# Performance work log

Measured on AMD Instinct MI355X. Metric: run time of the kernel, lower is better.

## Reference

```python
import jax, jax.numpy as jnp
import numpy as np

EMBED = 768
HEADS = 12
HEAD_DIM = EMBED // HEADS
HIDDEN = 4 * EMBED
EPS = 1e-5


def setup_inputs() -> dict:
    key = jax.random.key(0)
    ks = jax.random.split(key, 12)
    s = lambda fan_in: 1.0 / np.sqrt(fan_in)
    return {
        "x": jax.random.normal(ks[0], (4, 2048, EMBED), dtype=jnp.float32),
        "ln1_g": jnp.ones((EMBED,), jnp.float32),
        "ln1_b": jnp.zeros((EMBED,), jnp.float32),
        "qkv_w": jax.random.normal(ks[1], (EMBED, 3 * EMBED), jnp.float32) * s(EMBED),
        "qkv_b": jnp.zeros((3 * EMBED,), jnp.float32),
        "proj_w": jax.random.normal(ks[2], (EMBED, EMBED), jnp.float32) * s(EMBED),
        "proj_b": jnp.zeros((EMBED,), jnp.float32),
        "ln2_g": jnp.ones((EMBED,), jnp.float32),
        "ln2_b": jnp.zeros((EMBED,), jnp.float32),
        "fc1_w": jax.random.normal(ks[3], (EMBED, HIDDEN), jnp.float32) * s(EMBED),
        "fc1_b": jnp.zeros((HIDDEN,), jnp.float32),
        "fc2_w": jax.random.normal(ks[4], (HIDDEN, EMBED), jnp.float32) * s(HIDDEN),
        "fc2_b": jnp.zeros((EMBED,), jnp.float32),
    }


def _layernorm(x, g, b):
    mu = jnp.mean(x, axis=-1, keepdims=True)
    var = jnp.var(x, axis=-1, keepdims=True)
    return (x - mu) * jax.lax.rsqrt(var + EPS) * g + b


def reference(x, ln1_g, ln1_b, qkv_w, qkv_b, proj_w, proj_b,
              ln2_g, ln2_b, fc1_w, fc1_b, fc2_w, fc2_b):
    B, N, C = x.shape
    # --- attention (pre-LN) ---
    xn = _layernorm(x, ln1_g, ln1_b)
    qkv = xn @ qkv_w + qkv_b                       # [B,N,3C]
    qkv = qkv.reshape(B, N, 3, HEADS, HEAD_DIM)
    q, k, v = jnp.moveaxis(qkv, 2, 0)              # each [B,N,H,D]
    q = jnp.swapaxes(q, 1, 2)                      # [B,H,N,D]
    k = jnp.swapaxes(k, 1, 2)
    v = jnp.swapaxes(v, 1, 2)
    scale = HEAD_DIM ** -0.5
    attn = jax.nn.softmax(jnp.einsum('bhnd,bhmd->bhnm', q, k) * scale, axis=-1)
    out = jnp.einsum('bhnm,bhmd->bhnd', attn, v)   # [B,H,N,D]
    out = jnp.swapaxes(out, 1, 2).reshape(B, N, C)
    out = out @ proj_w + proj_b
    x = x + out
    # --- MLP (pre-LN) ---
    xn2 = _layernorm(x, ln2_g, ln2_b)
    h = jax.nn.gelu(xn2 @ fc1_w + fc1_b, approximate=False)
    x = x + (h @ fc2_w + fc2_b)
    return x
```

## Files before the change

kernel.cpp:

```cpp
#include <hip/hip_runtime.h>

typedef unsigned short ushort_t;
typedef __attribute__((ext_vector_type(8))) unsigned short ushort8;
typedef __attribute__((ext_vector_type(4))) unsigned short ushort4v;
typedef __attribute__((ext_vector_type(2))) unsigned int uint2v;
typedef __attribute__((ext_vector_type(4))) float f32x4;
typedef __attribute__((ext_vector_type(8))) __bf16 bf16x8;

#define DEVFN static __device__ __forceinline__

DEVFN unsigned short f2bf(float f) {
    unsigned int u = __builtin_bit_cast(unsigned int, f);
    u += 0x7FFFu + ((u >> 16) & 1u);
    return (unsigned short)(u >> 16);
}

DEVFN bf16x8 ldsfrag(const ushort_t* p) {
    ushort8 u = *reinterpret_cast<const ushort8*>(p);
    return __builtin_bit_cast(bf16x8, u);
}

DEVFN bf16x8 ldg8(const ushort_t* p) {
    ushort8 u = *reinterpret_cast<const ushort8*>(p);
    return __builtin_bit_cast(bf16x8, u);
}

DEVFN f32x4 mfma16(bf16x8 a, bf16x8 b, f32x4 c) {
    return __builtin_amdgcn_mfma_f32_16x16x32_bf16(a, b, c, 0, 0, 0);
}

DEVFN void gl2lds16(const ushort_t* g, ushort_t* l) {
    __builtin_amdgcn_global_load_lds(
        (const __attribute__((address_space(1))) unsigned int*)g,
        (__attribute__((address_space(3))) unsigned int*)l, 16, 0, 0);
}

DEVFN unsigned int cvtpk(float lo, float hi) {
    unsigned int r;
    asm("v_cvt_pk_bf16_f32 %0, %1, %2" : "=v"(r) : "v"(lo), "v"(hi));
    return r;
}

__global__ __launch_bounds__(256) void wt_kernel(const float* __restrict__ in,
                                                 ushort_t* __restrict__ out,
                                                 int K, int N) {
    __shared__ float t[32][33];
    const int n0 = blockIdx.x * 32, k0 = blockIdx.y * 32;
    const int tx = threadIdx.x & 31, ty = threadIdx.x >> 5;
    for (int j = 0; j < 4; j++)
        t[ty + 8 * j][tx] = in[(size_t)(k0 + ty + 8 * j) * N + n0 + tx];
    __syncthreads();
    for (int j = 0; j < 4; j++)
        out[(size_t)(n0 + ty + 8 * j) * K + k0 + tx] = f2bf(t[tx][ty + 8 * j]);
}

__global__ __launch_bounds__(256) void ln_kernel(const float* __restrict__ x,
                                                 const float* __restrict__ g,
                                                 const float* __restrict__ bta,
                                                 ushort_t* __restrict__ out) {
    const int row = blockIdx.x;
    const int tid = threadIdx.x;
    const float* xr = x + (size_t)row * 768;
    float v0 = xr[tid], v1 = xr[tid + 256], v2 = xr[tid + 512];
    float s = v0 + v1 + v2;
    float q = v0 * v0 + v1 * v1 + v2 * v2;
    for (int d = 32; d; d >>= 1) {
        s += __shfl_down(s, d);
        q += __shfl_down(q, d);
    }
    __shared__ float red[8];
    const int w = tid >> 6, lane = tid & 63;
    if (lane == 0) { red[w] = s; red[4 + w] = q; }
    __syncthreads();
    if (tid == 0) {
        float ts = red[0] + red[1] + red[2] + red[3];
        float tq = red[4] + red[5] + red[6] + red[7];
        float mu = ts * (1.0f / 768.0f);
        float var = tq * (1.0f / 768.0f) - mu * mu;
        red[0] = mu;
        red[1] = rsqrtf(var + 1e-5f);
    }
    __syncthreads();
    const float mu = red[0], rs = red[1];
    ushort_t* orow = out + (size_t)row * 768;
    orow[tid]       = f2bf((v0 - mu) * rs * g[tid]       + bta[tid]);
    orow[tid + 256] = f2bf((v1 - mu) * rs * g[tid + 256] + bta[tid + 256]);
    orow[tid + 512] = f2bf((v2 - mu) * rs * g[tid + 512] + bta[tid + 512]);
}

enum { EPI_QKV = 0, EPI_RES = 1, EPI_GELU = 2 };

template <int EPI, int BN>
__global__ __launch_bounds__(256) void gemm_kernel(
    const ushort_t* __restrict__ A, const ushort_t* __restrict__ BT,
    const float* __restrict__ bias, const float* __restrict__ resid,
    float* __restrict__ outf, ushort_t* __restrict__ outb,
    ushort_t* __restrict__ vtout, int M, int N, int K) {
    constexpr int NT = BN / 32;
    constexpr int BIW = BN / 32;
    __shared__ __align__(16) ushort_t As[128 * 64];
    __shared__ __align__(16) ushort_t Bs[BN * 64];
    const int bn = blockIdx.x, bm = blockIdx.y;
    const int tid = threadIdx.x;
    const int lane = tid & 63, w = tid >> 6;
    const int wm = (w >> 1) * 64, wn = (w & 1) * (BN / 2);
    const int l15 = lane & 15, l4 = lane >> 4;

    const int srow8 = lane >> 3;
    const int scol = ((lane & 7) ^ srow8) * 8;

    const ushort_t* gA = A + (size_t)(bm * 128 + w * 32 + srow8) * K + scol;
    ushort_t* lA = As + (w * 32) * 64;
    const ushort_t* gB = BT + (size_t)(bn * BN + w * (BN / 4) + srow8) * K + scol;
    ushort_t* lB = Bs + (w * (BN / 4)) * 64;

    const int sw7 = l15 & 7;
    const int aoff0 = (wm + l15) * 64 + ((l4 ^ sw7) * 8);
    const int aoff1 = (wm + l15) * 64 + (((4 + l4) ^ sw7) * 8);
    const int boff0 = (wn + l15) * 64 + ((l4 ^ sw7) * 8);
    const int boff1 = (wn + l15) * 64 + (((4 + l4) ^ sw7) * 8);

    f32x4 acc[4][NT] = {};

    for (int k0 = 0; k0 < K; k0 += 64) {
        __syncthreads();
#pragma unroll
        for (int i = 0; i < 4; i++)
            gl2lds16(gA + k0 + (size_t)i * 8 * K, lA + i * 512);
#pragma unroll
        for (int i = 0; i < BIW; i++)
            gl2lds16(gB + k0 + (size_t)i * 8 * K, lB + i * 512);
        __syncthreads();
#pragma unroll
        for (int kk = 0; kk < 2; kk++) {
            const int ao = kk ? aoff1 : aoff0;
            const int bo = kk ? boff1 : boff0;
            bf16x8 af[4], bfr[NT];
#pragma unroll
            for (int mt = 0; mt < 4; mt++)
                af[mt] = ldsfrag(As + ao + mt * 1024);
#pragma unroll
            for (int nt = 0; nt < NT; nt++)
                bfr[nt] = ldsfrag(Bs + bo + nt * 1024);
#pragma unroll
            for (int mt = 0; mt < 4; mt++)
#pragma unroll
                for (int nt = 0; nt < NT; nt++)
                    acc[mt][nt] = mfma16(bfr[nt], af[mt], acc[mt][nt]);
        }
    }

#pragma unroll
    for (int nt = 0; nt < NT; nt++) {
        const int gc0 = bn * BN + wn + nt * 16 + l4 * 4;
        const f32x4 bi = *reinterpret_cast<const f32x4*>(bias + gc0);
#pragma unroll
        for (int mt = 0; mt < 4; mt++) {
            const int gr = bm * 128 + wm + mt * 16 + l15;
            f32x4 v = acc[mt][nt] + bi;
            if constexpr (EPI == EPI_QKV) {
                if (gc0 < 768) v *= 0.18033688011f;
                if (gc0 >= 1536) {
                    const int d = gc0 - 1536;
                    const int h = d >> 6, dh = d & 63;
                    const int b = gr >> 11, tl = gr & 2047;
                    ushort_t* vrow = vtout + ((size_t)((b * 12 + h) * 64 + dh)) * 2048 + tl;
                    vrow[0]        = f2bf(v[0]);
                    vrow[2048]     = f2bf(v[1]);
                    vrow[2 * 2048] = f2bf(v[2]);
                    vrow[3 * 2048] = f2bf(v[3]);
                } else {
                    ushort4v o;
#pragma unroll
                    for (int r = 0; r < 4; r++) o[r] = f2bf(v[r]);
                    *reinterpret_cast<ushort4v*>(outb + (size_t)gr * N + gc0) = o;
                }
            } else if constexpr (EPI == EPI_RES) {
                const f32x4 rsd = *reinterpret_cast<const f32x4*>(resid + (size_t)gr * N + gc0);
                *reinterpret_cast<f32x4*>(outf + (size_t)gr * N + gc0) = v + rsd;
            } else {
                ushort4v o;
#pragma unroll
                for (int r = 0; r < 4; r++) {
                    const float gl = 0.5f * v[r] * (1.0f + erff(v[r] * 0.70710678118f));
                    o[r] = f2bf(gl);
                }
                *reinterpret_cast<ushort4v*>(outb + (size_t)gr * N + gc0) = o;
            }
        }
    }
}

__global__ __launch_bounds__(256, 4) void attn_kernel(const ushort_t* __restrict__ qkv,
                                                      const ushort_t* __restrict__ vt,
                                                      ushort_t* __restrict__ out) {
    __shared__ __align__(16) ushort_t Kb[2][4096];
    __shared__ __align__(16) ushort_t Vb[2][4096];
    __shared__ __align__(16) ushort_t Ps[4][1024];

    const int bid = blockIdx.x;
    const int nid = (bid & 7) * 192 + (bid >> 3);
    const int qt = nid & 31;
    const int bh = nid >> 5;
    const int b = bh / 12, h = bh % 12;
    const int tid = threadIdx.x;
    const int lane = tid & 63, w = tid >> 6;
    const int l15 = lane & 15, l4 = lane >> 4;

    const ushort_t* qrow = qkv + (size_t)(b * 2048 + qt * 64 + w * 16 + l15) * 2304 + h * 64;
    const bf16x8 aq0 = ldg8(qrow + l4 * 8);
    const bf16x8 aq1 = ldg8(qrow + 32 + l4 * 8);

    const int jr0 = w * 16 + (lane >> 3);
    const int jr1 = jr0 + 8;
    const int c0 = ((lane & 7) ^ (jr0 & 7)) * 8;
    const int c1 = ((lane & 7) ^ (jr1 & 7)) * 8;
    const ushort_t* kg0 = qkv + (size_t)(b * 2048 + jr0) * 2304 + 768 + h * 64 + c0;
    const ushort_t* kg1 = qkv + (size_t)(b * 2048 + jr1) * 2304 + 768 + h * 64 + c1;
    const ushort_t* vg0 = vt + (size_t)(bh * 64 + jr0) * 2048 + c0;
    const ushort_t* vg1 = vt + (size_t)(bh * 64 + jr1) * 2048 + c1;

    const int sw7 = l15 & 7;
    const int ka0 = l15 * 64 + ((l4 ^ sw7) * 8);
    const int ka1 = l15 * 64 + (((4 + l4) ^ sw7) * 8);

    ushort_t* const psw = Ps[w];
    const int pw_m = l15 & 14;
    int pwoff[4];
#pragma unroll
    for (int jt = 0; jt < 4; jt++) pwoff[jt] = l15 * 64 + (((jt * 4 + l4) ^ pw_m) * 4);
    const int pr0 = l15 * 64 + (((2 * l4) ^ pw_m) * 4);
    const int pr1 = l15 * 64 + (((8 + 2 * l4) ^ pw_m) * 4);

    float lrun = 0.f;
    f32x4 oacc[4] = {};

    gl2lds16(kg0, &Kb[0][w * 1024]);
    gl2lds16(kg1, &Kb[0][w * 1024 + 512]);
    gl2lds16(vg0, &Vb[0][w * 1024]);
    gl2lds16(vg1, &Vb[0][w * 1024 + 512]);
    __syncthreads();

    for (int kt = 0; kt < 32; kt++) {
        const int cur = kt & 1;
        if (kt < 31) {
            const size_t ko = (size_t)(kt + 1) * 64 * 2304;
            const int vo = (kt + 1) * 64;
            gl2lds16(kg0 + ko, &Kb[cur ^ 1][w * 1024]);
            gl2lds16(kg1 + ko, &Kb[cur ^ 1][w * 1024 + 512]);
            gl2lds16(vg0 + vo, &Vb[cur ^ 1][w * 1024]);
            gl2lds16(vg1 + vo, &Vb[cur ^ 1][w * 1024 + 512]);
        }
        const ushort_t* kb = Kb[cur];
        const ushort_t* vb = Vb[cur];

        f32x4 st[4];
        __builtin_amdgcn_s_setprio(1);
#pragma unroll
        for (int jt = 0; jt < 4; jt++) {
            f32x4 z = {};
            z = mfma16(ldsfrag(kb + ka0 + jt * 1024), aq0, z);
            z = mfma16(ldsfrag(kb + ka1 + jt * 1024), aq1, z);
            st[jt] = z;
        }
        __builtin_amdgcn_s_setprio(0);

        float rs = 0.f;
#pragma unroll
        for (int jt = 0; jt < 4; jt++) {
            const float p0 = __builtin_amdgcn_exp2f(st[jt][0]);
            const float p1 = __builtin_amdgcn_exp2f(st[jt][1]);
            const float p2 = __builtin_amdgcn_exp2f(st[jt][2]);
            const float p3 = __builtin_amdgcn_exp2f(st[jt][3]);
            rs += (p0 + p1) + (p2 + p3);
            uint2v pw;
            pw[0] = cvtpk(p0, p1);
            pw[1] = cvtpk(p2, p3);
            *reinterpret_cast<uint2v*>(psw + pwoff[jt]) = pw;
        }
        lrun += rs;

        const bf16x8 pf0 = ldsfrag(psw + pr0);
        const bf16x8 pf1 = ldsfrag(psw + pr1);

        __builtin_amdgcn_s_setprio(1);
#pragma unroll
        for (int dt = 0; dt < 4; dt++) {
            const bf16x8 vf0 = ldsfrag(vb + ka0 + dt * 1024);
            const bf16x8 vf1 = ldsfrag(vb + ka1 + dt * 1024);
            oacc[dt] = mfma16(vf0, pf0, oacc[dt]);
            oacc[dt] = mfma16(vf1, pf1, oacc[dt]);
        }
        __builtin_amdgcn_s_setprio(0);
        __syncthreads();
    }

    lrun += __shfl_xor(lrun, 16);
    lrun += __shfl_xor(lrun, 32);
    const float linv = __builtin_amdgcn_rcpf(lrun);

    ushort_t* orow = out + (size_t)(b * 2048 + qt * 64 + w * 16 + l15) * 768 + h * 64 + l4 * 4;
#pragma unroll
    for (int dt = 0; dt < 4; dt++) {
        ushort4v o;
#pragma unroll
        for (int r = 0; r < 4; r++) o[r] = f2bf(oacc[dt][r] * linv);
        *reinterpret_cast<ushort4v*>(orow + dt * 16) = o;
    }
}

extern "C" void kernel_launch(void* const* d_in, const int* in_sizes, int n_in,
                              void* d_out, int out_size, void* d_ws, size_t ws_size,
                              hipStream_t stream) {
    const float* x      = (const float*)d_in[0];
    const float* ln1_g  = (const float*)d_in[1];
    const float* ln1_b  = (const float*)d_in[2];
    const float* qkv_w  = (const float*)d_in[3];
    const float* qkv_b  = (const float*)d_in[4];
    const float* proj_w = (const float*)d_in[5];
    const float* proj_b = (const float*)d_in[6];
    const float* ln2_g  = (const float*)d_in[7];
    const float* ln2_b  = (const float*)d_in[8];
    const float* fc1_w  = (const float*)d_in[9];
    const float* fc1_b  = (const float*)d_in[10];
    const float* fc2_w  = (const float*)d_in[11];
    const float* fc2_b  = (const float*)d_in[12];
    float* out = (float*)d_out;

    char* ws = (char*)d_ws;
    ushort_t* qkv_wt  = (ushort_t*)(ws);
    ushort_t* proj_wt = (ushort_t*)(ws + 3538944);
    ushort_t* fc1_wt  = (ushort_t*)(ws + 4718592);
    ushort_t* fc2_wt  = (ushort_t*)(ws + 9437184);
    ushort_t* xb      = (ushort_t*)(ws + 14155776);
    ushort_t* aob     = (ushort_t*)(ws + 26738688);
    ushort_t* qkvb    = (ushort_t*)(ws + 39321600);
    ushort_t* vtb     = (ushort_t*)(ws + 77070336);
    ushort_t* hb      = (ushort_t*)(ws + 39321600);

    dim3 blk(256);

    wt_kernel<<<dim3(72, 24), blk, 0, stream>>>(qkv_w, qkv_wt, 768, 2304);
    wt_kernel<<<dim3(24, 24), blk, 0, stream>>>(proj_w, proj_wt, 768, 768);
    wt_kernel<<<dim3(96, 24), blk, 0, stream>>>(fc1_w, fc1_wt, 768, 3072);
    wt_kernel<<<dim3(24, 96), blk, 0, stream>>>(fc2_w, fc2_wt, 3072, 768);

    ln_kernel<<<8192, blk, 0, stream>>>(x, ln1_g, ln1_b, xb);
    gemm_kernel<EPI_QKV, 128><<<dim3(18, 64), blk, 0, stream>>>(
        xb, qkv_wt, qkv_b, nullptr, nullptr, qkvb, vtb, 8192, 2304, 768);
    attn_kernel<<<dim3(1536), blk, 0, stream>>>(qkvb, vtb, aob);
    gemm_kernel<EPI_RES, 64><<<dim3(12, 64), blk, 0, stream>>>(
        aob, proj_wt, proj_b, x, out, nullptr, nullptr, 8192, 768, 768);
    ln_kernel<<<8192, blk, 0, stream>>>(out, ln2_g, ln2_b, xb);
    gemm_kernel<EPI_GELU, 128><<<dim3(24, 64), blk, 0, stream>>>(
        xb, fc1_wt, fc1_b, nullptr, nullptr, hb, nullptr, 8192, 3072, 768);
    gemm_kernel<EPI_RES, 64><<<dim3(12, 64), blk, 0, stream>>>(
        hb, fc2_wt, fc2_b, out, out, nullptr, nullptr, 8192, 768, 3072);
}
```

Baseline: 315.5 us.

## Double-buffer GEMM LDS tiles, fuse weight transposes, use fast GELU and packed bf16 stores

The GEMM kernel now keeps two LDS stages and issues the next k-tile's global-to-LDS loads before computing the current one, so memory latency can overlap with MFMA work. BK becomes a template parameter, set to 32 for the wide GEMMs to limit LDS use. The four weight-transpose launches are merged into one kernel to cut launch overhead. The GELU epilogue switches from erf to a tanh approximation built from exp2/rcp, and bf16 stores use packed hardware conversion. The tanh GELU changes numerics slightly relative to the exact erf reference.

```diff
diff --git a/kernel.cpp b/kernel.cpp
--- a/kernel.cpp
+++ b/kernel.cpp
@@ -41,11 +41,32 @@
     return r;
 }
 
-__global__ __launch_bounds__(256) void wt_kernel(const float* __restrict__ in,
-                                                 ushort_t* __restrict__ out,
-                                                 int K, int N) {
+DEVFN float gelu_fast(float v) {
+    const float a = 0.7978845608f * v * fmaf(0.044715f, v * v, 1.0f);
+    const float e = __builtin_amdgcn_exp2f(2.885390082f * a);
+    const float th = 1.0f - 2.0f * __builtin_amdgcn_rcpf(e + 1.0f);
+    return 0.5f * v * (1.0f + th);
+}
+
+__global__ __launch_bounds__(256) void wt4_kernel(
+    const float* __restrict__ qkv_w, const float* __restrict__ proj_w,
+    const float* __restrict__ fc1_w, const float* __restrict__ fc2_w,
+    ushort_t* __restrict__ qkv_wt, ushort_t* __restrict__ proj_wt,
+    ushort_t* __restrict__ fc1_wt, ushort_t* __restrict__ fc2_wt) {
     __shared__ float t[32][33];
-    const int n0 = blockIdx.x * 32, k0 = blockIdx.y * 32;
+    const int bid = blockIdx.x;
+    const float* in; ushort_t* out; int K, N, n0, k0;
+    if (bid < 1728)      { in = qkv_w;  out = qkv_wt;  K = 768;  N = 2304;
+                           n0 = (bid % 72) * 32;  k0 = (bid / 72) * 32; }
+    else if (bid < 2304) { const int r = bid - 1728; in = proj_w; out = proj_wt;
+                           K = 768;  N = 768;
+                           n0 = (r % 24) * 32;    k0 = (r / 24) * 32; }
+    else if (bid < 4608) { const int r = bid - 2304; in = fc1_w;  out = fc1_wt;
+                           K = 768;  N = 3072;
+                           n0 = (r % 96) * 32;    k0 = (r / 96) * 32; }
+    else                 { const int r = bid - 4608; in = fc2_w;  out = fc2_wt;
+                           K = 3072; N = 768;
+                           n0 = (r % 24) * 32;    k0 = (r / 24) * 32; }
     const int tx = threadIdx.x & 31, ty = threadIdx.x >> 5;
     for (int j = 0; j < 4; j++)
         t[ty + 8 * j][tx] = in[(size_t)(k0 + ty + 8 * j) * N + n0 + tx];
@@ -90,64 +111,72 @@
 
 enum { EPI_QKV = 0, EPI_RES = 1, EPI_GELU = 2 };
 
-template <int EPI, int BN>
+template <int EPI, int BN, int BK>
 __global__ __launch_bounds__(256) void gemm_kernel(
     const ushort_t* __restrict__ A, const ushort_t* __restrict__ BT,
     const float* __restrict__ bias, const float* __restrict__ resid,
     float* __restrict__ outf, ushort_t* __restrict__ outb,
     ushort_t* __restrict__ vtout, int M, int N, int K) {
     constexpr int NT = BN / 32;
-    constexpr int BIW = BN / 32;
-    __shared__ __align__(16) ushort_t As[128 * 64];
-    __shared__ __align__(16) ushort_t Bs[BN * 64];
+    constexpr int SL = BK / 8;
+    constexpr int SM = SL - 1;
+    constexpr int RPI = 64 / SL;
+    constexpr int AI = 128 / RPI / 4;
+    constexpr int BI = BN / RPI / 4;
+    __shared__ __align__(16) ushort_t As[2][128 * BK];
+    __shared__ __align__(16) ushort_t Bs[2][BN * BK];
     const int bn = blockIdx.x, bm = blockIdx.y;
     const int tid = threadIdx.x;
     const int lane = tid & 63, w = tid >> 6;
     const int wm = (w >> 1) * 64, wn = (w & 1) * (BN / 2);
     const int l15 = lane & 15, l4 = lane >> 4;
 
-    const int srow8 = lane >> 3;
-    const int scol = ((lane & 7) ^ srow8) * 8;
-
-    const ushort_t* gA = A + (size_t)(bm * 128 + w * 32 + srow8) * K + scol;
-    ushort_t* lA = As + (w * 32) * 64;
-    const ushort_t* gB = BT + (size_t)(bn * BN + w * (BN / 4) + srow8) * K + scol;
-    ushort_t* lB = Bs + (w * (BN / 4)) * 64;
-
-    const int sw7 = l15 & 7;
-    const int aoff0 = (wm + l15) * 64 + ((l4 ^ sw7) * 8);
-    const int aoff1 = (wm + l15) * 64 + (((4 + l4) ^ sw7) * 8);
-    const int boff0 = (wn + l15) * 64 + ((l4 ^ sw7) * 8);
-    const int boff1 = (wn + l15) * 64 + (((4 + l4) ^ sw7) * 8);
+    const int srow = lane / SL;
+    const int scol = ((lane & SM) ^ (srow & SM)) * 8;
+    const ushort_t* gA = A + (size_t)(bm * 128 + w * (AI * RPI) + srow) * K + scol;
+    const ushort_t* gB = BT + (size_t)(bn * BN + w * (BI * RPI) + srow) * K + scol;
+
+    const int swm = l15 & SM;
+    int aoff[BK / 32], boff[BK / 32];
+#pragma unroll
+    for (int kk = 0; kk < BK / 32; kk++) {
+        aoff[kk] = (wm + l15) * BK + ((((kk << 2) | l4) ^ swm) * 8);
+        boff[kk] = (wn + l15) * BK + ((((kk << 2) | l4) ^ swm) * 8);
+    }
 
     f32x4 acc[4][NT] = {};
 
-    for (int k0 = 0; k0 < K; k0 += 64) {
-        __syncthreads();
-#pragma unroll
-        for (int i = 0; i < 4; i++)
-            gl2lds16(gA + k0 + (size_t)i * 8 * K, lA + i * 512);
-#pragma unroll
-        for (int i = 0; i < BIW; i++)
-            gl2lds16(gB + k0 + (size_t)i * 8 * K, lB + i * 512);
-        __syncthreads();
-#pragma unroll
-        for (int kk = 0; kk < 2; kk++) {
-            const int ao = kk ? aoff1 : aoff0;
-            const int bo = kk ? boff1 : boff0;
+    auto stage = [&](int k0, int buf) {
+#pragma unroll
+        for (int i = 0; i < AI; i++)
+            gl2lds16(gA + k0 + i * RPI * K, &As[buf][(w * AI + i) * 512]);
+#pragma unroll
+        for (int i = 0; i < BI; i++)
+            gl2lds16(gB + k0 + i * RPI * K, &Bs[buf][(w * BI + i) * 512]);
+    };
+
+    stage(0, 0);
+    __syncthreads();
+    int cur = 0;
+    for (int k0 = 0; k0 < K; k0 += BK) {
+        if (k0 + BK < K) stage(k0 + BK, cur ^ 1);
+#pragma unroll
+        for (int kk = 0; kk < BK / 32; kk++) {
             bf16x8 af[4], bfr[NT];
 #pragma unroll
             for (int mt = 0; mt < 4; mt++)
-                af[mt] = ldsfrag(As + ao + mt * 1024);
+                af[mt] = ldsfrag(As[cur] + aoff[kk] + mt * 16 * BK);
 #pragma unroll
             for (int nt = 0; nt < NT; nt++)
-                bfr[nt] = ldsfrag(Bs + bo + nt * 1024);
+                bfr[nt] = ldsfrag(Bs[cur] + boff[kk] + nt * 16 * BK);
 #pragma unroll
             for (int mt = 0; mt < 4; mt++)
 #pragma unroll
                 for (int nt = 0; nt < NT; nt++)
                     acc[mt][nt] = mfma16(bfr[nt], af[mt], acc[mt][nt]);
         }
+        __syncthreads();
+        cur ^= 1;
     }
 
 #pragma unroll
@@ -170,22 +199,22 @@
                     vrow[2 * 2048] = f2bf(v[2]);
                     vrow[3 * 2048] = f2bf(v[3]);
                 } else {
-                    ushort4v o;
-#pragma unroll
-                    for (int r = 0; r < 4; r++) o[r] = f2bf(v[r]);
-                    *reinterpret_cast<ushort4v*>(outb + (size_t)gr * N + gc0) = o;
+                    uint2v o;
+                    o[0] = cvtpk(v[0], v[1]);
+                    o[1] = cvtpk(v[2], v[3]);
+                    *reinterpret_cast<uint2v*>(outb + (size_t)gr * N + gc0) = o;
                 }
             } else if constexpr (EPI == EPI_RES) {
                 const f32x4 rsd = *reinterpret_cast<const f32x4*>(resid + (size_t)gr * N + gc0);
                 *reinterpret_cast<f32x4*>(outf + (size_t)gr * N + gc0) = v + rsd;
             } else {
-                ushort4v o;
-#pragma unroll
-                for (int r = 0; r < 4; r++) {
-                    const float gl = 0.5f * v[r] * (1.0f + erff(v[r] * 0.70710678118f));
-                    o[r] = f2bf(gl);
-                }
-                *reinterpret_cast<ushort4v*>(outb + (size_t)gr * N + gc0) = o;
+                f32x4 gl;
+#pragma unroll
+                for (int r = 0; r < 4; r++) gl[r] = gelu_fast(v[r]);
+                uint2v o;
+                o[0] = cvtpk(gl[0], gl[1]);
+                o[1] = cvtpk(gl[2], gl[3]);
+                *reinterpret_cast<uint2v*>(outb + (size_t)gr * N + gc0) = o;
             }
         }
     }
@@ -340,20 +369,17 @@
 
     dim3 blk(256);
 
-    wt_kernel<<<dim3(72, 24), blk, 0, stream>>>(qkv_w, qkv_wt, 768, 2304);
-    wt_kernel<<<dim3(24, 24), blk, 0, stream>>>(proj_w, proj_wt, 768, 768);
-    wt_kernel<<<dim3(96, 24), blk, 0, stream>>>(fc1_w, fc1_wt, 768, 3072);
-    wt_kernel<<<dim3(24, 96), blk, 0, stream>>>(fc2_w, fc2_wt, 3072, 768);
-
+    wt4_kernel<<<dim3(6912), blk, 0, stream>>>(qkv_w, proj_w, fc1_w, fc2_w,
+                                               qkv_wt, proj_wt, fc1_wt, fc2_wt);
     ln_kernel<<<8192, blk, 0, stream>>>(x, ln1_g, ln1_b, xb);
-    gemm_kernel<EPI_QKV, 128><<<dim3(18, 64), blk, 0, stream>>>(
+    gemm_kernel<EPI_QKV, 128, 32><<<dim3(18, 64), blk, 0, stream>>>(
         xb, qkv_wt, qkv_b, nullptr, nullptr, qkvb, vtb, 8192, 2304, 768);
     attn_kernel<<<dim3(1536), blk, 0, stream>>>(qkvb, vtb, aob);
-    gemm_kernel<EPI_RES, 64><<<dim3(12, 64), blk, 0, stream>>>(
+    gemm_kernel<EPI_RES, 64, 64><<<dim3(12, 64), blk, 0, stream>>>(
         aob, proj_wt, proj_b, x, out, nullptr, nullptr, 8192, 768, 768);
     ln_kernel<<<8192, blk, 0, stream>>>(out, ln2_g, ln2_b, xb);
-    gemm_kernel<EPI_GELU, 128><<<dim3(24, 64), blk, 0, stream>>>(
+    gemm_kernel<EPI_GELU, 128, 32><<<dim3(24, 64), blk, 0, stream>>>(
         xb, fc1_wt, fc1_b, nullptr, nullptr, hb, nullptr, 8192, 3072, 768);
-    gemm_kernel<EPI_RES, 64><<<dim3(12, 64), blk, 0, stream>>>(
+    gemm_kernel<EPI_RES, 64, 64><<<dim3(12, 64), blk, 0, stream>>>(
         hb, fc2_wt, fc2_b, out, out, nullptr, nullptr, 8192, 768, 3072);
 }
```

After: 313.8 us. About the same (-0.6%).
